# Performance work log

Hardware: AMD Instinct MI355X
Metric: run time of the kernel (lower is better)

The kernel has to match this reference:

```python
import jax, jax.numpy as jnp
import numpy as np

BLOCK = 256


def setup_inputs() -> dict:
    key = jax.random.key(0)
    ks = jax.random.split(key, 6)
    b, n, hid = 2, 4096, 2048
    h, d = 16, 128
    x = jax.random.normal(ks[0], (b, n, hid), dtype=jnp.float32)
    slope_rate = jax.random.uniform(ks[1], (h, 1, 1), dtype=jnp.float32)
    Wqkv = jax.random.normal(ks[2], (3 * h * d, hid), dtype=jnp.float32) * 0.02
    Wg = jax.random.normal(ks[3], (h * d, hid), dtype=jnp.float32) * 0.02
    norm_w = jnp.ones((h * d,), dtype=jnp.float32)
    Wo = jax.random.normal(ks[4], (hid, h * d), dtype=jnp.float32) * 0.02
    return {"x": x, "slope_rate": slope_rate, "Wqkv": Wqkv, "Wg": Wg, "norm_w": norm_w, "Wo": Wo}


def reference(x, slope_rate, Wqkv, Wg, norm_w, Wo):
    b, n, hid = x.shape
    h = slope_rate.shape[0]
    d = Wqkv.shape[0] // (3 * h)
    nb = n // BLOCK

    qkv = jax.nn.silu(x @ Wqkv.T).reshape(b, n, h, 3 * d)
    q, k, v = jnp.split(qkv, 3, axis=-1)           # each (b, n, h, d)
    # -> (b, h, n, d)
    q = q.transpose(0, 2, 1, 3)
    k = k.transpose(0, 2, 1, 3)
    v = v.transpose(0, 2, 1, 3)

    s = slope_rate.astype(jnp.float32)             # (h, 1, 1)
    arr = jnp.arange(1, BLOCK + 1, dtype=jnp.float32)
    q_decay = jnp.exp(-s * arr[:, None])           # (h, BLOCK, 1)
    k_decay = jnp.exp(-s * (BLOCK - arr[:, None])) # (h, BLOCK, 1)
    idx = arr[:, None] - arr[None, :]              # (BLOCK, BLOCK)
    diag_decay = jnp.where(idx >= 0, jnp.exp(-s * idx), 0.0)  # (h, BLOCK, BLOCK)
    block_decay = jnp.exp(-s * BLOCK)              # (h, 1, 1)

    # chunk into blocks: (nb, b, h, BLOCK, d)
    def chunk(t):
        return t.reshape(b, h, nb, BLOCK, d).transpose(2, 0, 1, 3, 4)
    qc, kc, vc = chunk(q), chunk(k), chunk(v)

    def step(kv, qkv_blk):
        qi, ki, vi = qkv_blk
        # inter-block: decayed query against running kv state
        out_nd = jnp.einsum('bhmd,bhde->bhme', qi * q_decay, kv)
        # intra-block: decay-masked quadratic attention
        qk = jnp.einsum('bhmd,bhnd->bhmn', qi, ki) * diag_decay
        out_d = jnp.einsum('bhmn,bhne->bhme', qk, vi)
        kv_new = block_decay * kv + jnp.einsum('bhmd,bhme->bhde', ki * k_decay, vi)
        return kv_new, out_nd + out_d

    kv0 = jnp.zeros((b, h, d, d), dtype=jnp.float32)
    _, out_blocks = jax.lax.scan(step, kv0, (qc, kc, vc))  # (nb, b, h, BLOCK, d)

    out = out_blocks.transpose(1, 2, 0, 3, 4).reshape(b, h, n, d)
    out = out.transpose(0, 2, 1, 3).reshape(b, n, h * d)  # b n (h d)

    # RMSNorm
    eps = jnp.finfo(jnp.float32).eps
    rms = jax.lax.rsqrt(jnp.mean(out * out, axis=-1, keepdims=True) + eps)
    out = out * rms * norm_w

    gate = jax.nn.sigmoid(x @ Wg.T)
    return (gate * out) @ Wo.T
```

## Files before the change

kernel.cpp:

```cpp
#include <hip/hip_runtime.h>
#include <stdint.h>

typedef __attribute__((ext_vector_type(8))) short short8;
typedef __attribute__((ext_vector_type(4))) float f32x4;

#define DEV static __device__ __forceinline__

DEV float b2f(unsigned short u) {
  unsigned x = ((unsigned)u) << 16;
  return __builtin_bit_cast(float, x);
}
DEV unsigned short f2b(float f) {
  unsigned x = __builtin_bit_cast(unsigned, f);
  return (unsigned short)((x + 0x7fffu + ((x >> 16) & 1u)) >> 16);
}
DEV void gload16(const unsigned short* g, unsigned short* l) {
  __builtin_amdgcn_global_load_lds((const __attribute__((address_space(1))) void*)g,
                                   (__attribute__((address_space(3))) void*)l, 16, 0, 0);
}
#define MFMA(a, b, c) __builtin_amdgcn_mfma_f32_16x16x32_bf16(a, b, c, 0, 0, 0)
#define BARRIER                          \
  asm volatile("" ::: "memory");         \
  __builtin_amdgcn_s_barrier();          \
  asm volatile("" ::: "memory")

__global__ void k_f2b(const float* __restrict__ in, unsigned short* __restrict__ out, long n) {
  long i = ((long)blockIdx.x * blockDim.x + threadIdx.x) * 4;
  long stride = (long)gridDim.x * blockDim.x * 4;
  for (; i < n; i += stride) {
    float4 f = *(const float4*)(in + i);
    ushort4 o;
    o.x = f2b(f.x); o.y = f2b(f.y); o.z = f2b(f.z); o.w = f2b(f.w);
    *(ushort4*)(out + i) = o;
  }
}

#define LDFRAG(dst, base, posbase)                                                        \
  {                                                                                       \
    _Pragma("unroll") for (int fi = 0; fi < 4; ++fi) {                                    \
      int pos = (posbase) + fi * 16 + l15;                                                \
      _Pragma("unroll") for (int ks = 0; ks < 2; ++ks)                                    \
          dst[fi][ks] =                                                                   \
              *(const short8*)((base) + pos * 64 + (((ks * 4 + l4) ^ (pos & 7)) << 3));   \
    }                                                                                     \
  }

template <int MODE>
__global__ __launch_bounds__(512, 2) void k_gemm(
    const unsigned short* __restrict__ A, const unsigned short* __restrict__ B0,
    const unsigned short* __restrict__ B1,
    unsigned short* __restrict__ o_q, unsigned short* __restrict__ o_k,
    unsigned short* __restrict__ o_v, unsigned short* __restrict__ o_g,
    float* __restrict__ o_f) {
  const int K = 2048, NT = 32;
  __shared__ unsigned short sm[65536];
  int tid = threadIdx.x, w = tid >> 6, lane = tid & 63;
  int wm = w >> 2, wn = w & 3;
  int l15 = lane & 15, l4 = lane >> 4;
  int xcd = blockIdx.x & 7, sub = blockIdx.x >> 3;
  int tm = xcd * 4 + (sub & 3), tn = sub >> 2;
  int brow = tm << 8, bcol = tn << 8;
  const unsigned short* Ab = A + (size_t)brow * K;
  const unsigned short* Bb = (MODE == 1 || bcol < 6144) ? (B0 + (size_t)bcol * K)
                                                        : (B1 + (size_t)(bcol - 6144) * K);
  f32x4 acc[8][4];
#pragma unroll
  for (int m = 0; m < 8; m++)
#pragma unroll
    for (int n = 0; n < 4; n++) acc[m][n] = (f32x4)0.f;

  auto stageU = [&](int TT, int s) {
    int tsrc = TT < NT ? TT : NT - 1;
    unsigned short* lb = sm + (TT & 1) * 32768 + s * 8192;
    int kt = tsrc << 6;
    const unsigned short* gb = (s & 1) ? Bb : Ab;
    int ro = (s >> 1) << 7;
#pragma unroll
    for (int i = 0; i < 2; ++i) {
      int c = i * 512 + tid;
      int pos = c >> 3, pb = c & 7;
      gload16(gb + (size_t)(ro + pos) * K + kt + ((pb ^ (pos & 7)) << 3), lb + c * 8);
    }
  };

  const int bslot = (wn >> 1) ? 3 : 1;
  const int bposb = (wn & 1) * 64;
  short8 afA[4][2], afB[4][2], bfr[4][2];

  stageU(0, 0); stageU(0, 1); stageU(0, 3); stageU(0, 2);
  asm volatile("s_waitcnt vmcnt(2)" ::: "memory");
  BARRIER;
  LDFRAG(afA, sm, wm * 64);
  stageU(1, 0); stageU(1, 1); stageU(1, 3);
  asm volatile("s_waitcnt vmcnt(6)" ::: "memory");
  BARRIER;

  for (int T = 0; T < NT; ++T) {
    const unsigned short* buf0 = sm + (T & 1) * 32768;
    const unsigned short* buf1 = sm + ((T + 1) & 1) * 32768;
    LDFRAG(bfr, buf0 + bslot * 8192, bposb);
    LDFRAG(afB, buf0 + 2 * 8192, wm * 64);
    stageU(T + 1, 2);
    __builtin_amdgcn_s_setprio(1);
#pragma unroll
    for (int mi = 0; mi < 4; ++mi)
#pragma unroll
      for (int nj = 0; nj < 4; ++nj)
#pragma unroll
        for (int ks = 0; ks < 2; ++ks) acc[mi][nj] = MFMA(afA[mi][ks], bfr[nj][ks], acc[mi][nj]);
    __builtin_amdgcn_s_setprio(0);
    asm volatile("s_waitcnt vmcnt(2)" ::: "memory");
    BARRIER;
    LDFRAG(afA, buf1, wm * 64);
    stageU(T + 2, 0); stageU(T + 2, 1); stageU(T + 2, 3);
    __builtin_amdgcn_s_setprio(1);
#pragma unroll
    for (int mi = 0; mi < 4; ++mi)
#pragma unroll
      for (int nj = 0; nj < 4; ++nj)
#pragma unroll
        for (int ks = 0; ks < 2; ++ks)
          acc[4 + mi][nj] = MFMA(afB[mi][ks], bfr[nj][ks], acc[4 + mi][nj]);
    __builtin_amdgcn_s_setprio(0);
    asm volatile("s_waitcnt vmcnt(6)" ::: "memory");
    BARRIER;
  }

#pragma unroll
  for (int mf = 0; mf < 8; ++mf)
#pragma unroll
    for (int r = 0; r < 4; ++r) {
      int row = brow + (mf >> 2) * 128 + wm * 64 + (mf & 3) * 16 + l4 * 4 + r;
#pragma unroll
      for (int ni = 0; ni < 4; ++ni) {
        int col = bcol + wn * 64 + ni * 16 + l15;
        float v = acc[mf][ni][r];
        if (MODE == 0) {
          if (col < 6144) {
            float sv = v / (1.f + __expf(-v));
            int h = col / 384, dd = col - h * 384;
            int b = row >> 12, t = row & 4095;
            size_t base = ((size_t)(b * 16 + h) * 4096 + t) * 128;
            if (dd < 128) o_q[base + dd] = f2b(sv);
            else if (dd < 256) o_k[base + dd - 128] = f2b(sv);
            else o_v[base + dd - 256] = f2b(sv);
          } else {
            float gv = 1.f / (1.f + __expf(-v));
            o_g[(size_t)row * 2048 + (col - 6144)] = f2b(gv);
          }
        } else {
          o_f[(size_t)row * 2048 + col] = v;
        }
      }
    }
}

__global__ __launch_bounds__(256) void k_kvblk(const unsigned short* __restrict__ kk,
                                               const unsigned short* __restrict__ vv,
                                               const float* __restrict__ slope,
                                               unsigned short* __restrict__ kvT) {
  int gid = blockIdx.x;
  int bh = gid >> 4, blk = gid & 15;
  float s = slope[bh & 15];
  __shared__ unsigned short kT[128][72];
  __shared__ unsigned short vT[128][72];
  int tid = threadIdx.x, w = tid >> 6, lane = tid & 63;
  int wrow = (w >> 1) * 64, wcol = (w & 1) * 64;
  f32x4 acc[4][4];
#pragma unroll
  for (int m = 0; m < 4; m++)
#pragma unroll
    for (int n = 0; n < 4; n++) acc[m][n] = (f32x4)0.f;
  const unsigned short* kb = kk + ((size_t)bh * 4096 + blk * 256) * 128;
  const unsigned short* vb = vv + ((size_t)bh * 4096 + blk * 256) * 128;
  int tt = tid & 63, c0 = (tid >> 6) * 32;
  for (int tc = 0; tc < 4; ++tc) {
    __syncthreads();
    int tg = tc * 64 + tt;
    float kd = __expf(-s * (float)(255 - tg));
#pragma unroll
    for (int g = 0; g < 4; ++g) {
      int c = c0 + g * 8;
      short8 k8 = *(const short8*)(kb + (size_t)tg * 128 + c);
      short8 v8 = *(const short8*)(vb + (size_t)tg * 128 + c);
#pragma unroll
      for (int j = 0; j < 8; ++j) {
        kT[c + j][tt] = f2b(b2f((unsigned short)k8[j]) * kd);
        vT[c + j][tt] = (unsigned short)v8[j];
      }
    }
    __syncthreads();
#pragma unroll
    for (int kx = 0; kx < 64; kx += 32) {
      int ko = kx + (lane >> 4) * 8;
      short8 af[4], bfr[4];
#pragma unroll
      for (int m = 0; m < 4; m++) af[m] = *(const short8*)&vT[wrow + m * 16 + (lane & 15)][ko];
#pragma unroll
      for (int n = 0; n < 4; n++) bfr[n] = *(const short8*)&kT[wcol + n * 16 + (lane & 15)][ko];
#pragma unroll
      for (int m = 0; m < 4; m++)
#pragma unroll
        for (int n = 0; n < 4; n++) acc[m][n] = MFMA(af[m], bfr[n], acc[m][n]);
    }
  }
  unsigned short* op = kvT + (size_t)gid * 16384;
#pragma unroll
  for (int m = 0; m < 4; m++)
#pragma unroll
    for (int r = 0; r < 4; r++) {
      int e = wrow + m * 16 + (lane >> 4) * 4 + r;
#pragma unroll
      for (int n = 0; n < 4; n++) {
        int d = wcol + n * 16 + (lane & 15);
        op[e * 128 + d] = f2b(acc[m][n][r]);
      }
    }
}

__global__ void k_scan(unsigned short* kvT, const float* __restrict__ slope) {
  int gid = blockIdx.x;
  int bh = gid >> 6;
  int eo = (gid & 63) * 256 + threadIdx.x;
  float s = slope[bh & 15];
  float bd = __expf(-s * 256.f);
  float st = 0.f;
  size_t base = (size_t)bh * 16 * 16384 + eo;
#pragma unroll
  for (int i = 0; i < 16; ++i) {
    unsigned short c = kvT[base + (size_t)i * 16384];
    kvT[base + (size_t)i * 16384] = f2b(st);
    st = bd * st + b2f(c);
  }
}

__global__ __launch_bounds__(256) void k_attn(const unsigned short* __restrict__ q,
                                              const unsigned short* __restrict__ kk,
                                              const unsigned short* __restrict__ vv,
                                              const unsigned short* __restrict__ kvT,
                                              const float* __restrict__ slope,
                                              unsigned short* __restrict__ attn) {
  int gid = blockIdx.x;
  int hf = gid & 1, blk = (gid >> 1) & 15, bh = gid >> 5;
  float s = slope[bh & 15];
  __shared__ unsigned short k_sh[64][136];
  __shared__ unsigned short vT_sh[128][72];
  __shared__ unsigned short s_sh[4][32][72];
  int tid = threadIdx.x, w = tid >> 6, lane = tid & 63;
  int mm0 = hf * 128 + w * 32;
  const unsigned short* qb = q + ((size_t)bh * 4096 + blk * 256) * 128;
  const unsigned short* kvb = kvT + (size_t)(bh * 16 + blk) * 16384;
  f32x4 acc[2][8];
#pragma unroll
  for (int m = 0; m < 2; m++)
#pragma unroll
    for (int n = 0; n < 8; n++) acc[m][n] = (f32x4)0.f;
#pragma unroll
  for (int kx = 0; kx < 128; kx += 32) {
    int ko = kx + (lane >> 4) * 8;
    short8 af[2], bfr[8];
#pragma unroll
    for (int mi = 0; mi < 2; mi++)
      af[mi] = *(const short8*)(qb + (size_t)(mm0 + mi * 16 + (lane & 15)) * 128 + ko);
#pragma unroll
    for (int ni = 0; ni < 8; ni++)
      bfr[ni] = *(const short8*)(kvb + (size_t)(ni * 16 + (lane & 15)) * 128 + ko);
#pragma unroll
    for (int mi = 0; mi < 2; mi++)
#pragma unroll
      for (int ni = 0; ni < 8; ni++) acc[mi][ni] = MFMA(af[mi], bfr[ni], acc[mi][ni]);
  }
#pragma unroll
  for (int mi = 0; mi < 2; mi++)
#pragma unroll
    for (int r = 0; r < 4; r++) {
      float qd = __expf(-s * (float)(mm0 + mi * 16 + (lane >> 4) * 4 + r + 1));
#pragma unroll
      for (int ni = 0; ni < 8; ni++) acc[mi][ni][r] *= qd;
    }
  int nchunk = 2 * (hf + 1);
  for (int tc = 0; tc < nchunk; ++tc) {
    __syncthreads();
    {
      int t2 = tid >> 2, c = (tid & 3) * 32;
      const unsigned short* kp = kk + ((size_t)bh * 4096 + blk * 256 + tc * 64 + t2) * 128 + c;
#pragma unroll
      for (int g = 0; g < 4; ++g) *(short8*)&k_sh[t2][c + g * 8] = *(const short8*)(kp + g * 8);
    }
    {
      int t2 = tid & 63, e0 = (tid >> 6) * 32;
      const unsigned short* vp = vv + ((size_t)bh * 4096 + blk * 256 + tc * 64 + t2) * 128 + e0;
#pragma unroll
      for (int g = 0; g < 4; ++g) {
        short8 v8 = *(const short8*)(vp + g * 8);
#pragma unroll
        for (int j = 0; j < 8; ++j) vT_sh[e0 + g * 8 + j][t2] = (unsigned short)v8[j];
      }
    }
    __syncthreads();
    if (tc * 64 <= mm0 + 31) {
      f32x4 sa[2][4];
#pragma unroll
      for (int m = 0; m < 2; m++)
#pragma unroll
        for (int n = 0; n < 4; n++) sa[m][n] = (f32x4)0.f;
#pragma unroll
      for (int kx = 0; kx < 128; kx += 32) {
        int ko = kx + (lane >> 4) * 8;
        short8 af[2], bfr[4];
#pragma unroll
        for (int mi = 0; mi < 2; mi++)
          af[mi] = *(const short8*)(qb + (size_t)(mm0 + mi * 16 + (lane & 15)) * 128 + ko);
#pragma unroll
        for (int ni = 0; ni < 4; ni++) bfr[ni] = *(const short8*)&k_sh[ni * 16 + (lane & 15)][ko];
#pragma unroll
        for (int mi = 0; mi < 2; mi++)
#pragma unroll
          for (int ni = 0; ni < 4; ni++) sa[mi][ni] = MFMA(af[mi], bfr[ni], sa[mi][ni]);
      }
#pragma unroll
      for (int mi = 0; mi < 2; mi++)
#pragma unroll
        for (int ni = 0; ni < 4; ni++)
#pragma unroll
          for (int r = 0; r < 4; r++) {
            int mm = mm0 + mi * 16 + (lane >> 4) * 4 + r;
            int ttg = tc * 64 + ni * 16 + (lane & 15);
            int diff = mm - ttg;
            float val = (diff >= 0) ? sa[mi][ni][r] * __expf(-s * (float)diff) : 0.f;
            s_sh[w][mi * 16 + (lane >> 4) * 4 + r][ni * 16 + (lane & 15)] = f2b(val);
          }
#pragma unroll
      for (int k2 = 0; k2 < 64; k2 += 32) {
        int ko2 = k2 + (lane >> 4) * 8;
        short8 a2[2];
#pragma unroll
        for (int mi = 0; mi < 2; mi++)
          a2[mi] = *(const short8*)&s_sh[w][mi * 16 + (lane & 15)][ko2];
#pragma unroll
        for (int ni = 0; ni < 8; ni++) {
          short8 b2 = *(const short8*)&vT_sh[ni * 16 + (lane & 15)][ko2];
#pragma unroll
          for (int mi = 0; mi < 2; mi++) acc[mi][ni] = MFMA(a2[mi], b2, acc[mi][ni]);
        }
      }
    }
  }
  int b = bh >> 4, h = bh & 15;
#pragma unroll
  for (int mi = 0; mi < 2; mi++)
#pragma unroll
    for (int r = 0; r < 4; r++) {
      int mm = mm0 + mi * 16 + (lane >> 4) * 4 + r;
      size_t rowp = ((size_t)b * 4096 + blk * 256 + mm) * 2048 + h * 128;
#pragma unroll
      for (int ni = 0; ni < 8; ni++) attn[rowp + ni * 16 + (lane & 15)] = f2b(acc[mi][ni][r]);
    }
}

__global__ __launch_bounds__(256) void k_norm(const unsigned short* __restrict__ attn,
                                              const unsigned short* __restrict__ gate,
                                              const float* __restrict__ nw,
                                              unsigned short* __restrict__ y) {
  int row = blockIdx.x;
  int tid = threadIdx.x, w = tid >> 6, lane = tid & 63;
  const unsigned short* ap = attn + (size_t)row * 2048 + tid * 8;
  const unsigned short* gp = gate + (size_t)row * 2048 + tid * 8;
  short8 a8 = *(const short8*)ap;
  float vals[8];
  float ss = 0.f;
#pragma unroll
  for (int j = 0; j < 8; ++j) {
    vals[j] = b2f((unsigned short)a8[j]);
    ss += vals[j] * vals[j];
  }
#pragma unroll
  for (int off = 32; off > 0; off >>= 1) ss += __shfl_down(ss, off, 64);
  __shared__ float red[4];
  if (lane == 0) red[w] = ss;
  __syncthreads();
  float tot = red[0] + red[1] + red[2] + red[3];
  float rms = rsqrtf(tot * (1.f / 2048.f) + 1.1920929e-07f);
  short8 g8 = *(const short8*)gp;
  short8 o;
#pragma unroll
  for (int j = 0; j < 8; ++j)
    o[j] = (short)f2b(vals[j] * rms * nw[tid * 8 + j] * b2f((unsigned short)g8[j]));
  *(short8*)(y + (size_t)row * 2048 + tid * 8) = o;
}

extern "C" void kernel_launch(void* const* d_in, const int* in_sizes, int n_in, void* d_out,
                              int out_size, void* d_ws, size_t ws_size, hipStream_t stream) {
  const float* x = (const float*)d_in[0];
  const float* slope = (const float*)d_in[1];
  const float* Wqkv = (const float*)d_in[2];
  const float* Wg = (const float*)d_in[3];
  const float* nw = (const float*)d_in[4];
  const float* Wo = (const float*)d_in[5];
  float* out = (float*)d_out;

  unsigned short* q = (unsigned short*)d_ws;
  unsigned short* k = q + 16777216;
  unsigned short* v = k + 16777216;
  unsigned short* gate = v + 16777216;
  unsigned short* xb = gate + 16777216;
  unsigned short* wqkvb = xb + 16777216;
  unsigned short* wgb = wqkvb + 12582912;
  unsigned short* wob = wgb + 4194304;
  unsigned short* kvT = wob + 4194304;
  unsigned short* attn = wqkvb;
  unsigned short* y = xb;

  k_f2b<<<2048, 256, 0, stream>>>(x, xb, 16777216L);
  k_f2b<<<2048, 256, 0, stream>>>(Wqkv, wqkvb, 12582912L);
  k_f2b<<<1024, 256, 0, stream>>>(Wg, wgb, 4194304L);
  k_f2b<<<1024, 256, 0, stream>>>(Wo, wob, 4194304L);

  k_gemm<0><<<1024, 512, 0, stream>>>(xb, wqkvb, wgb, q, k, v, gate, nullptr);
  k_kvblk<<<512, 256, 0, stream>>>(k, v, slope, kvT);
  k_scan<<<2048, 256, 0, stream>>>(kvT, slope);
  k_attn<<<1024, 256, 0, stream>>>(q, k, v, kvT, slope, attn);
  k_norm<<<8192, 256, 0, stream>>>(attn, gate, nw, y);
  k_gemm<1><<<256, 512, 0, stream>>>(y, wob, nullptr, nullptr, nullptr, nullptr, nullptr, out);
}
```

Before: 512.9 us.

## Restructure GEMM main loop with precomputed LDS offsets and shallower prefetch

The main GEMM loop is rewritten so that LDS fragment offsets and global source pointers are computed once before the loop; each stage then just bumps its pointer by one K tile. The prefetch schedule changes from staging tiles two iterations ahead with register-double-buffered A fragments to a simpler one-tile-ahead scheme that reloads A fragments per half. The goal is to cut per-iteration address arithmetic and register pressure. The cost is a shorter lead between global loads and their use, which may expose latency. The clamp on the last tile is dropped, so the final iteration loads one tile past the K range into an unused buffer.

```diff
diff --git a/kernel.cpp b/kernel.cpp
--- a/kernel.cpp
+++ b/kernel.cpp
@@ -34,16 +34,6 @@
     *(ushort4*)(out + i) = o;
   }
 }
-
-#define LDFRAG(dst, base, posbase)                                                        \
-  {                                                                                       \
-    _Pragma("unroll") for (int fi = 0; fi < 4; ++fi) {                                    \
-      int pos = (posbase) + fi * 16 + l15;                                                \
-      _Pragma("unroll") for (int ks = 0; ks < 2; ++ks)                                    \
-          dst[fi][ks] =                                                                   \
-              *(const short8*)((base) + pos * 64 + (((ks * 4 + l4) ^ (pos & 7)) << 3));   \
-    }                                                                                     \
-  }
 
 template <int MODE>
 __global__ __launch_bounds__(512, 2) void k_gemm(
@@ -69,60 +59,85 @@
 #pragma unroll
     for (int n = 0; n < 4; n++) acc[m][n] = (f32x4)0.f;
 
-  auto stageU = [&](int TT, int s) {
-    int tsrc = TT < NT ? TT : NT - 1;
-    unsigned short* lb = sm + (TT & 1) * 32768 + s * 8192;
-    int kt = tsrc << 6;
-    const unsigned short* gb = (s & 1) ? Bb : Ab;
-    int ro = (s >> 1) << 7;
+  int rdA[4][2], rdB[4][2];
+  const int bslot = (wn >> 1) ? 3 : 1;
+  const int bposb = (wn & 1) * 64;
+#pragma unroll
+  for (int fi = 0; fi < 4; ++fi) {
+#pragma unroll
+    for (int ks = 0; ks < 2; ++ks) {
+      int posA = wm * 64 + fi * 16 + l15;
+      rdA[fi][ks] = posA * 128 + (((ks * 4 + l4) ^ (posA & 7)) << 4);
+      int posB = bposb + fi * 16 + l15;
+      rdB[fi][ks] = bslot * 16384 + posB * 128 + (((ks * 4 + l4) ^ (posB & 7)) << 4);
+    }
+  }
+  const unsigned short* gP[4][2];
+  int dL[4][2];
+#pragma unroll
+  for (int s = 0; s < 4; ++s) {
 #pragma unroll
     for (int i = 0; i < 2; ++i) {
       int c = i * 512 + tid;
       int pos = c >> 3, pb = c & 7;
-      gload16(gb + (size_t)(ro + pos) * K + kt + ((pb ^ (pos & 7)) << 3), lb + c * 8);
+      const unsigned short* gb = (s & 1) ? Bb : Ab;
+      int ro = (s >> 1) << 7;
+      gP[s][i] = gb + (size_t)(ro + pos) * K + ((pb ^ (pos & 7)) << 3);
+      dL[s][i] = s * 16384 + c * 16;
+    }
+  }
+
+  auto stage = [&](int s, int tgl) {
+#pragma unroll
+    for (int i = 0; i < 2; ++i) {
+      gload16(gP[s][i], (unsigned short*)((char*)sm + (dL[s][i] + tgl)));
+      gP[s][i] += 64;
     }
   };
 
-  const int bslot = (wn >> 1) ? 3 : 1;
-  const int bposb = (wn & 1) * 64;
-  short8 afA[4][2], afB[4][2], bfr[4][2];
-
-  stageU(0, 0); stageU(0, 1); stageU(0, 3); stageU(0, 2);
+  stage(0, 0); stage(1, 0); stage(3, 0); stage(2, 0);
   asm volatile("s_waitcnt vmcnt(2)" ::: "memory");
   BARRIER;
-  LDFRAG(afA, sm, wm * 64);
-  stageU(1, 0); stageU(1, 1); stageU(1, 3);
-  asm volatile("s_waitcnt vmcnt(6)" ::: "memory");
-  BARRIER;
 
   for (int T = 0; T < NT; ++T) {
-    const unsigned short* buf0 = sm + (T & 1) * 32768;
-    const unsigned short* buf1 = sm + ((T + 1) & 1) * 32768;
-    LDFRAG(bfr, buf0 + bslot * 8192, bposb);
-    LDFRAG(afB, buf0 + 2 * 8192, wm * 64);
-    stageU(T + 1, 2);
+    const char* smb = (const char*)sm + ((T & 1) << 16);
+    int tglS = ((T + 1) & 1) << 16;
+    short8 af[4][2], bfr[4][2];
+#pragma unroll
+    for (int nj = 0; nj < 4; ++nj)
+#pragma unroll
+      for (int ks = 0; ks < 2; ++ks) bfr[nj][ks] = *(const short8*)(smb + rdB[nj][ks]);
+#pragma unroll
+    for (int fi = 0; fi < 4; ++fi)
+#pragma unroll
+      for (int ks = 0; ks < 2; ++ks) af[fi][ks] = *(const short8*)(smb + rdA[fi][ks]);
+    stage(0, tglS); stage(1, tglS); stage(3, tglS);
     __builtin_amdgcn_s_setprio(1);
 #pragma unroll
     for (int mi = 0; mi < 4; ++mi)
 #pragma unroll
       for (int nj = 0; nj < 4; ++nj)
 #pragma unroll
-        for (int ks = 0; ks < 2; ++ks) acc[mi][nj] = MFMA(afA[mi][ks], bfr[nj][ks], acc[mi][nj]);
+        for (int ks = 0; ks < 2; ++ks) acc[mi][nj] = MFMA(af[mi][ks], bfr[nj][ks], acc[mi][nj]);
+    __builtin_amdgcn_s_setprio(0);
+    asm volatile("s_waitcnt vmcnt(6)" ::: "memory");
+    BARRIER;
+#pragma unroll
+    for (int fi = 0; fi < 4; ++fi)
+#pragma unroll
+      for (int ks = 0; ks < 2; ++ks)
+        af[fi][ks] = *(const short8*)(smb + (rdA[fi][ks] + 32768));
+    stage(2, tglS);
+    __builtin_amdgcn_s_setprio(1);
+#pragma unroll
+    for (int mi = 0; mi < 4; ++mi)
+#pragma unroll
+      for (int nj = 0; nj < 4; ++nj)
+#pragma unroll
+        for (int ks = 0; ks < 2; ++ks)
+          acc[4 + mi][nj] = MFMA(af[mi][ks], bfr[nj][ks], acc[4 + mi][nj]);
     __builtin_amdgcn_s_setprio(0);
     asm volatile("s_waitcnt vmcnt(2)" ::: "memory");
-    BARRIER;
-    LDFRAG(afA, buf1, wm * 64);
-    stageU(T + 2, 0); stageU(T + 2, 1); stageU(T + 2, 3);
-    __builtin_amdgcn_s_setprio(1);
-#pragma unroll
-    for (int mi = 0; mi < 4; ++mi)
-#pragma unroll
-      for (int nj = 0; nj < 4; ++nj)
-#pragma unroll
-        for (int ks = 0; ks < 2; ++ks)
-          acc[4 + mi][nj] = MFMA(afB[mi][ks], bfr[nj][ks], acc[4 + mi][nj]);
-    __builtin_amdgcn_s_setprio(0);
-    asm volatile("s_waitcnt vmcnt(6)" ::: "memory");
     BARRIER;
   }
 
```

Result: no change. 507.0 us (-1.1%).
